# Optimization experiments

Measured on AMD Instinct MI355X. Metric: run time of the kernel, lower is better.

## Reference

```python
import jax, jax.numpy as jnp
import numpy as np

NUM_EXPERTS = 8
POWER_LAW_EXPONENT = 3.0


def setup_inputs() -> dict:
    key = jax.random.key(0)
    x = jax.random.normal(key, (32768, 1024), dtype=jnp.float32)
    return {"x": x}


def reference(x):
    # Forward depends only on x.shape[0]; all values come from RNG sampling,
    # matching RandomGate.forward (torch RNG replaced by fixed jax keys).
    dim = x.shape[0]
    E = NUM_EXPERTS
    assert dim % E == 0
    k_rand, k_mult, k_pois, k_perm = jax.random.split(jax.random.key(42), 4)

    # power-law distribution over experts: p_e ~ e^{-3}
    exps = jnp.arange(1, E + 1, dtype=jnp.float32) ** (-POWER_LAW_EXPONENT)
    p = exps / jnp.sum(exps)                                   # [E]

    # vectorized replacement for the per-row Python loop:
    # multinomial(p, num_samples=E, replacement=True) for every row at once
    random_matrix = jax.random.uniform(k_rand, (dim, E), dtype=jnp.float32)
    sampled = jax.random.categorical(k_mult, jnp.log(p), shape=(dim, E))   # [dim, E] int
    rates = jnp.take_along_axis(random_matrix, sampled, axis=1)            # [dim, E]
    pois = jax.random.poisson(k_pois, rates).astype(jnp.float32)           # [dim, E]

    # scatter sampled poisson values into a zero logits matrix
    rows = jnp.arange(dim)[:, None]                                        # [dim, 1]
    logits = jnp.zeros((dim, E), dtype=jnp.float32).at[rows, sampled].set(pois)

    # random_gating: softmax -> argmax -> one_hot -> random column permutation -> column sums
    gates = jax.nn.softmax(logits, axis=1)
    indices1_s = jnp.argmax(gates, axis=1)                                 # [dim]
    mask1 = jax.nn.one_hot(indices1_s, E, dtype=jnp.int32)                 # [dim, E]
    perm = jax.random.permutation(k_perm, E)
    mask1 = mask1[:, perm]
    expert_selection = jnp.sum(mask1, axis=0)                              # [E] int counts
    return expert_selection
```

## Files before the change

kernel.cpp:

```cpp
#include <hip/hip_runtime.h>
#include <stdint.h>
#include <string.h>
#include <math.h>


#define DIM    32768
#define NCHAIN 48
#define BLOCKS 1024

struct P1 {
  uint32_t kr0, kr1;
  uint32_t km0, km1;
  uint32_t sub0[NCHAIN];
  uint32_t sub1[NCHAIN];
  float    invp[8];
};
struct P2 { int invperm[8]; };

__host__ __device__ static inline void tf2x32(uint32_t k0, uint32_t k1,
                                              uint32_t x0, uint32_t x1,
                                              uint32_t &o0, uint32_t &o1) {
  const uint32_t ks2 = 0x1BD11BDAu ^ k0 ^ k1;
  x0 += k0; x1 += k1;
#define RL(v,s) (((v) << (s)) | ((v) >> (32 - (s))))
#define RND(r) { x0 += x1; x1 = RL(x1, r); x1 ^= x0; }
  RND(13) RND(15) RND(26) RND(6)
  x0 += k1;  x1 += ks2 + 1u;
  RND(17) RND(29) RND(16) RND(24)
  x0 += ks2; x1 += k0 + 2u;
  RND(13) RND(15) RND(26) RND(6)
  x0 += k0;  x1 += k1 + 3u;
  RND(17) RND(29) RND(16) RND(24)
  x0 += k1;  x1 += ks2 + 4u;
  RND(13) RND(15) RND(26) RND(6)
  x0 += ks2; x1 += k0 + 5u;
#undef RND
#undef RL
  o0 = x0; o1 = x1;
}

__device__ static inline uint32_t rbits(uint32_t k0, uint32_t k1, uint32_t e) {
  uint32_t o0, o1;
  tf2x32(k0, k1, 0u, e, o0, o1);
  return o0 ^ o1;
}

__device__ static inline float u01(uint32_t bits) {
  return __uint_as_float((bits >> 9) | 0x3F800000u) - 1.0f;
}

__global__ void __launch_bounds__(256, 4)
gate_kernel(P1 P, unsigned long long* __restrict__ ws) {
  __shared__ int hist[8];
  if (threadIdx.x < 8) hist[threadIdx.x] = 0;
  __syncthreads();

  const uint32_t gid  = blockIdx.x * 256u + threadIdx.x;
  const uint32_t row8 = gid & ~7u;
  const int      j    = (int)(gid & 7u);
  const float TINY = 1.17549435e-38f;

  int bestk = 0; float best = 3.0e38f;
#pragma unroll
  for (int kk = 0; kk < 8; ++kk) {
    float f = u01(rbits(P.km0, P.km1, gid * 8u + (uint32_t)kk));
    float u = fmaxf(f, TINY);
    float w = -__logf(u);
    float v = w * P.invp[kk];
    if (v < best) { best = v; bestk = kk; }
  }

  float lam = u01(rbits(P.kr0, P.kr1, row8 + (uint32_t)bestk));

  int pvi = 0;
  if (lam > 0.0f) {
    float lp = 0.0f; int kcnt = 0;
#pragma unroll 1
    for (int t = 0; t < NCHAIN; ++t) {
      if (!(lp > -lam)) break;
      ++kcnt;
      lp += __logf(u01(rbits(P.sub0[t], P.sub1[t], gid)));
    }
    pvi = kcnt - 1;
  }

  uint32_t packed = (uint32_t)bestk | ((uint32_t)pvi << 3);
  int v = 0;
#pragma unroll
  for (int jp = 0; jp < 8; ++jp) {
    uint32_t pk = __shfl(packed, jp, 8);
    v = ((int)(pk & 7u) == j) ? (int)(pk >> 3) : v;
  }
  int am = j;
#pragma unroll
  for (int m = 1; m < 8; m <<= 1) {
    int ov = __shfl_xor(v,  m, 8);
    int oa = __shfl_xor(am, m, 8);
    if (ov > v || (ov == v && oa < am)) { v = ov; am = oa; }
  }
  if (j == 0) atomicAdd(&hist[am], 1);
  __syncthreads();

  if (threadIdx.x == 0) {
    unsigned long long pk = 0ull;
#pragma unroll
    for (int e = 0; e < 8; ++e)
      pk |= (unsigned long long)(uint32_t)hist[e] << (8 * e);
    ws[blockIdx.x] = pk;
  }
}

__global__ void __launch_bounds__(256)
reduce_kernel(P2 P, const unsigned long long* __restrict__ ws,
              int* __restrict__ out) {
  const int t = threadIdx.x;

  int s0=0,s1=0,s2=0,s3=0,s4=0,s5=0,s6=0,s7=0;
#pragma unroll
  for (int r = 0; r < 4; ++r) {
    unsigned long long v = ws[t + 256 * r];
    s0 += (int)((v      ) & 0xFFull);
    s1 += (int)((v >>  8) & 0xFFull);
    s2 += (int)((v >> 16) & 0xFFull);
    s3 += (int)((v >> 24) & 0xFFull);
    s4 += (int)((v >> 32) & 0xFFull);
    s5 += (int)((v >> 40) & 0xFFull);
    s6 += (int)((v >> 48) & 0xFFull);
    s7 += (int)((v >> 56) & 0xFFull);
  }
#pragma unroll
  for (int m = 1; m < 64; m <<= 1) {
    s0 += __shfl_xor(s0, m); s1 += __shfl_xor(s1, m);
    s2 += __shfl_xor(s2, m); s3 += __shfl_xor(s3, m);
    s4 += __shfl_xor(s4, m); s5 += __shfl_xor(s5, m);
    s6 += __shfl_xor(s6, m); s7 += __shfl_xor(s7, m);
  }
  __shared__ int part[4][8];
  if ((t & 63) == 0) {
    const int w = t >> 6;
    part[w][0]=s0; part[w][1]=s1; part[w][2]=s2; part[w][3]=s3;
    part[w][4]=s4; part[w][5]=s5; part[w][6]=s6; part[w][7]=s7;
  }
  __syncthreads();
  if (t < 8) {
    int tot = part[0][t] + part[1][t] + part[2][t] + part[3][t];
    out[P.invperm[t]] = tot;
  }
}

extern "C" void kernel_launch(void* const* d_in, const int* in_sizes, int n_in,
                              void* d_out, int out_size, void* d_ws, size_t ws_size,
                              hipStream_t stream) {
  (void)d_in; (void)in_sizes; (void)n_in; (void)ws_size; (void)out_size;

  P1 P; P2 Q;

  uint32_t c0[4], c1[4];
  for (uint32_t i = 0; i < 4; ++i)
    tf2x32(0u, 42u, 0u, i, c0[i], c1[i]);
  P.kr0 = c0[0]; P.kr1 = c1[0];
  P.km0 = c0[1]; P.km1 = c1[1];
  uint32_t kp0 = c0[2], kp1 = c1[2];
  uint32_t kq0 = c0[3], kq1 = c1[3];

  {
    uint32_t r0 = kp0, r1 = kp1;
    for (int t = 0; t < NCHAIN; ++t) {
      uint32_t n0, n1, s0, s1;
      tf2x32(r0, r1, 0u, 0u, n0, n1);
      tf2x32(r0, r1, 0u, 1u, s0, s1);
      P.sub0[t] = s0; P.sub1[t] = s1;
      r0 = n0; r1 = n1;
    }
  }

  {
    uint32_t s0, s1;
    tf2x32(kq0, kq1, 0u, 1u, s0, s1);
    uint32_t sk[8];
    for (uint32_t i = 0; i < 8; ++i) {
      uint32_t a, b;
      tf2x32(s0, s1, 0u, i, a, b);
      sk[i] = a ^ b;
    }
    int perm[8]; bool used[8] = {false,false,false,false,false,false,false,false};
    for (int pos = 0; pos < 8; ++pos) {
      int best = -1;
      for (int i = 0; i < 8; ++i) {
        if (used[i]) continue;
        if (best < 0 || sk[i] < sk[best]) best = i;
      }
      used[best] = true; perm[pos] = best;
    }
    for (int i = 0; i < 8; ++i) Q.invperm[perm[i]] = i;
  }

  {
    float exps[8], Z = 0.0f;
    for (int e = 0; e < 8; ++e) { exps[e] = powf((float)(e + 1), -3.0f); Z += exps[e]; }
    for (int e = 0; e < 8; ++e) P.invp[e] = Z / exps[e];
  }

  int* out = (int*)d_out;
  unsigned long long* ws = (unsigned long long*)d_ws;
  gate_kernel<<<BLOCKS, 256, 0, stream>>>(P, ws);
  reduce_kernel<<<1, 256, 0, stream>>>(Q, ws, out);
}
```

Baseline: 16.90 us.

## Fuse histogram reduction into gate kernel via last-block flag spin-wait

Merges the separate single-block reduce kernel into the gate kernel. Each block publishes its packed histogram and then sets a per-block flag with a release store. The last block spins until every flag equals a magic value, then does the final reduction and writes the permuted output. This removes one kernel launch and the gap between the two launches. In exchange it relies on all blocks being co-resident to avoid deadlock. The flags are never reset, so on repeated calls stale flags can let the reducer read partials before they are rewritten.

```diff
diff --git a/kernel.cpp b/kernel.cpp
--- a/kernel.cpp
+++ b/kernel.cpp
@@ -7,6 +7,7 @@
 #define DIM    32768
 #define NCHAIN 48
 #define BLOCKS 1024
+#define MAGIC  0x5F3A9C71u
 
 struct P1 {
   uint32_t kr0, kr1;
@@ -50,7 +51,8 @@
 }
 
 __global__ void __launch_bounds__(256, 4)
-gate_kernel(P1 P, unsigned long long* __restrict__ ws) {
+fused_kernel(P1 P, P2 Q, unsigned long long* __restrict__ ws,
+             int* __restrict__ out) {
   __shared__ int hist[8];
   if (threadIdx.x < 8) hist[threadIdx.x] = 0;
   __syncthreads();
@@ -101,50 +103,67 @@
   if (j == 0) atomicAdd(&hist[am], 1);
   __syncthreads();
 
+  unsigned long long* partials = ws;
+  uint32_t*           flags    = (uint32_t*)(ws + BLOCKS);
+
   if (threadIdx.x == 0) {
     unsigned long long pk = 0ull;
 #pragma unroll
     for (int e = 0; e < 8; ++e)
       pk |= (unsigned long long)(uint32_t)hist[e] << (8 * e);
-    ws[blockIdx.x] = pk;
-  }
-}
-
-__global__ void __launch_bounds__(256)
-reduce_kernel(P2 P, const unsigned long long* __restrict__ ws,
-              int* __restrict__ out) {
-  const int t = threadIdx.x;
-
-  int s0=0,s1=0,s2=0,s3=0,s4=0,s5=0,s6=0,s7=0;
-#pragma unroll
-  for (int r = 0; r < 4; ++r) {
-    unsigned long long v = ws[t + 256 * r];
-    s0 += (int)((v      ) & 0xFFull);
-    s1 += (int)((v >>  8) & 0xFFull);
-    s2 += (int)((v >> 16) & 0xFFull);
-    s3 += (int)((v >> 24) & 0xFFull);
-    s4 += (int)((v >> 32) & 0xFFull);
-    s5 += (int)((v >> 40) & 0xFFull);
-    s6 += (int)((v >> 48) & 0xFFull);
-    s7 += (int)((v >> 56) & 0xFFull);
-  }
-#pragma unroll
-  for (int m = 1; m < 64; m <<= 1) {
-    s0 += __shfl_xor(s0, m); s1 += __shfl_xor(s1, m);
-    s2 += __shfl_xor(s2, m); s3 += __shfl_xor(s3, m);
-    s4 += __shfl_xor(s4, m); s5 += __shfl_xor(s5, m);
-    s6 += __shfl_xor(s6, m); s7 += __shfl_xor(s7, m);
-  }
-  __shared__ int part[4][8];
-  if ((t & 63) == 0) {
-    const int w = t >> 6;
-    part[w][0]=s0; part[w][1]=s1; part[w][2]=s2; part[w][3]=s3;
-    part[w][4]=s4; part[w][5]=s5; part[w][6]=s6; part[w][7]=s7;
-  }
-  __syncthreads();
-  if (t < 8) {
-    int tot = part[0][t] + part[1][t] + part[2][t] + part[3][t];
-    out[P.invperm[t]] = tot;
+    __hip_atomic_store(&partials[blockIdx.x], pk,
+                       __ATOMIC_RELAXED, __HIP_MEMORY_SCOPE_AGENT);
+    __hip_atomic_store(&flags[blockIdx.x], MAGIC,
+                       __ATOMIC_RELEASE, __HIP_MEMORY_SCOPE_AGENT);
+  }
+
+  if (blockIdx.x == BLOCKS - 1) {
+    const int t = threadIdx.x;
+    for (;;) {
+      bool done = true;
+#pragma unroll
+      for (int q = 0; q < 4; ++q) {
+        uint32_t f = __hip_atomic_load(&flags[t + q * 256],
+                                       __ATOMIC_RELAXED, __HIP_MEMORY_SCOPE_AGENT);
+        done &= (f == MAGIC);
+      }
+      if (__syncthreads_and((int)done)) break;
+      __builtin_amdgcn_s_sleep(1);
+    }
+    __threadfence();
+
+    int s0=0,s1=0,s2=0,s3=0,s4=0,s5=0,s6=0,s7=0;
+#pragma unroll
+    for (int r = 0; r < 4; ++r) {
+      unsigned long long pv = __hip_atomic_load(&partials[t + 256 * r],
+                                 __ATOMIC_RELAXED, __HIP_MEMORY_SCOPE_AGENT);
+      s0 += (int)((pv      ) & 0xFFull);
+      s1 += (int)((pv >>  8) & 0xFFull);
+      s2 += (int)((pv >> 16) & 0xFFull);
+      s3 += (int)((pv >> 24) & 0xFFull);
+      s4 += (int)((pv >> 32) & 0xFFull);
+      s5 += (int)((pv >> 40) & 0xFFull);
+      s6 += (int)((pv >> 48) & 0xFFull);
+      s7 += (int)((pv >> 56) & 0xFFull);
+    }
+#pragma unroll
+    for (int m = 1; m < 64; m <<= 1) {
+      s0 += __shfl_xor(s0, m); s1 += __shfl_xor(s1, m);
+      s2 += __shfl_xor(s2, m); s3 += __shfl_xor(s3, m);
+      s4 += __shfl_xor(s4, m); s5 += __shfl_xor(s5, m);
+      s6 += __shfl_xor(s6, m); s7 += __shfl_xor(s7, m);
+    }
+    __shared__ int part[4][8];
+    if ((t & 63) == 0) {
+      const int w = t >> 6;
+      part[w][0]=s0; part[w][1]=s1; part[w][2]=s2; part[w][3]=s3;
+      part[w][4]=s4; part[w][5]=s5; part[w][6]=s6; part[w][7]=s7;
+    }
+    __syncthreads();
+    if (t < 8) {
+      int tot = part[0][t] + part[1][t] + part[2][t] + part[3][t];
+      out[Q.invperm[t]] = tot;
+    }
   }
 }
 
@@ -203,6 +222,5 @@
 
   int* out = (int*)d_out;
   unsigned long long* ws = (unsigned long long*)d_ws;
-  gate_kernel<<<BLOCKS, 256, 0, stream>>>(P, ws);
-  reduce_kernel<<<1, 256, 0, stream>>>(Q, ws, out);
-}
+  fused_kernel<<<BLOCKS, 256, 0, stream>>>(P, Q, ws, out);
+}
```

Result: slower. 19.16 us (+13.4%).
